# Kernel tuning notes

Measured on AMD Instinct MI355X. Metric: run time of the kernel, lower is better.

## Reference

```python
import jax, jax.numpy as jnp
import numpy as np

SEARCH_RANGE = 4  # max_displacement; kernel_size=1, strides=1, pad=search_range
LEAKY_SLOPE = 0.1


def setup_inputs() -> dict:
    key = jax.random.key(0)
    k1, k2 = jax.random.split(key)
    B, H, W, C = 8, 128, 128, 192
    prv = jax.random.normal(k1, (B, H, W, C), dtype=jnp.float32)
    nxt = jax.random.normal(k2, (B, H, W, C), dtype=jnp.float32)
    return {"prv": prv, "nxt": nxt}


def _cost_volume(prv, nxt, d):
    # tfa CorrelationCost with kernel_size=1: for each displacement (dy, dx) in
    # [-d, d]^2, out[b,y,x,k] = mean_c prv[b,y,x,c] * nxt[b,y+dy,x+dx,c],
    # with zero padding of nxt by d. Displacements ordered row-major (dy outer).
    B, H, W, C = prv.shape
    nxt_p = jnp.pad(nxt, ((0, 0), (d, d), (d, d), (0, 0)))
    outs = []
    for dy in range(2 * d + 1):  # fixed small set (9)
        for dx in range(2 * d + 1):
            shifted = nxt_p[:, dy:dy + H, dx:dx + W, :]  # [B,H,W,C]
            outs.append(jnp.mean(prv * shifted, axis=-1))  # [B,H,W]
    return jnp.stack(outs, axis=-1)  # [B,H,W,81]


def reference(prv, nxt):
    cv = _cost_volume(prv, nxt, SEARCH_RANGE)
    return jax.nn.leaky_relu(cv, LEAKY_SLOPE)
```

## Files before the change

kernel.cpp:

```cpp
#include <hip/hip_runtime.h>
#include <hip/hip_bf16.h>


#define B_ 8
#define H_ 128
#define W_ 128
#define C_ 192
#define ND 9
#define NDISP 81
#define HT 16
#define WT 16
#define KS 32
#define NK 6
#define BROWS 24
#define BCOLS 24
#define APIX (HT * WT)
#define BPIX (BROWS * BCOLS)
#define ASTR 257
#define BSTR 577
#define ASLOTS (8 * ASTR)
#define BSLOTS (8 * BSTR)
#define NSA 2
#define NSB 5

typedef short short8 __attribute__((ext_vector_type(8)));
typedef short short4_t __attribute__((ext_vector_type(4)));
typedef float f32x4 __attribute__((ext_vector_type(4)));

static __device__ __forceinline__ short bf1(float f) {
    __hip_bfloat16 h = __float2bfloat16(f);
    return __builtin_bit_cast(short, h);
}

static __device__ __forceinline__ short4_t cvt4(float4 v) {
    short4_t r;
    r[0] = bf1(v.x); r[1] = bf1(v.y); r[2] = bf1(v.z); r[3] = bf1(v.w);
    return r;
}

static __device__ __forceinline__ short8 cat(short4_t u, short4_t v) {
    return __builtin_shufflevector(u, v, 0, 1, 2, 3, 4, 5, 6, 7);
}

static __device__ __forceinline__ void barrier_no_vm_drain() {
    asm volatile("s_waitcnt lgkmcnt(0)\n\ts_barrier" ::: "memory");
}

__global__ __launch_bounds__(1024, 4)
void cv_mfma(const float* __restrict__ prv, const float* __restrict__ nxt,
             float* __restrict__ out) {
    __shared__ short4_t sm[2][ASLOTS + BSLOTS];

    const int tid = threadIdx.x;
    const int w0 = blockIdx.x * WT;
    const int h0 = blockIdx.y * HT;
    const int b  = blockIdx.z;

    const int lane = tid & 63;
    const int wid  = tid >> 6;
    const int lq = lane & 15;
    const int lc = lane >> 4;

    const int tp = tid >> 3;
    const int c8 = tid & 7;

    int aoff[NSA];
#pragma unroll
    for (int i = 0; i < NSA; ++i) {
        const int p = tp + 128 * i;
        const int r = p >> 4;
        const int pc = p & 15;
        aoff[i] = ((b * H_ + h0 + r) * W_ + w0 + pc) * C_ + c8 * 4;
    }
    int boff[NSB];
    unsigned bmask = 0;
#pragma unroll
    for (int i = 0; i < NSB; ++i) {
        const int p = tp + 128 * i;
        const int row = p / BCOLS;
        const int col = p - row * BCOLS;
        const int gh = h0 - 4 + row;
        const int gw = w0 - 4 + col;
        const bool inb = (p < BPIX) && ((unsigned)gh < (unsigned)H_) && ((unsigned)gw < (unsigned)W_);
        if (inb) bmask |= (1u << i);
        boff[i] = ((b * H_ + (inb ? gh : 0)) * W_ + (inb ? gw : 0)) * C_ + c8 * 4;
    }
    const bool wr4 = (tid < 512);

    float4 xa[NSA], xb[NSB];

#pragma unroll
    for (int i = 0; i < NSA; ++i) xa[i] = *(const float4*)(prv + aoff[i]);
#pragma unroll
    for (int i = 0; i < NSB; ++i) {
        xb[i] = make_float4(0.f, 0.f, 0.f, 0.f);
        if (bmask & (1u << i)) xb[i] = *(const float4*)(nxt + boff[i]);
    }

    f32x4 acc[ND][2];
#pragma unroll
    for (int d = 0; d < ND; ++d) {
        acc[d][0] = (f32x4){0.f, 0.f, 0.f, 0.f};
        acc[d][1] = (f32x4){0.f, 0.f, 0.f, 0.f};
    }

    for (int it = 0; it < NK; ++it) {
        short4_t* sA = sm[it & 1];
        short4_t* sB = sm[it & 1] + ASLOTS;

#pragma unroll
        for (int i = 0; i < NSA; ++i)
            sA[c8 * ASTR + tp + 128 * i] = cvt4(xa[i]);
#pragma unroll
        for (int i = 0; i < NSB - 1; ++i)
            sB[c8 * BSTR + tp + 128 * i] = cvt4(xb[i]);
        if (wr4)
            sB[c8 * BSTR + tp + 128 * (NSB - 1)] = cvt4(xb[NSB - 1]);

        if (it + 1 < NK) {
            const int co = (it + 1) * KS;
#pragma unroll
            for (int i = 0; i < NSA; ++i) xa[i] = *(const float4*)(prv + aoff[i] + co);
#pragma unroll
            for (int i = 0; i < NSB; ++i) {
                if (bmask & (1u << i)) xb[i] = *(const float4*)(nxt + boff[i] + co);
            }
        }

        barrier_no_vm_drain();

        const int pA = wid * WT + lq;
        const short8 a = cat(sA[2 * lc * ASTR + pA], sA[(2 * lc + 1) * ASTR + pA]);
#pragma unroll
        for (int dy = 0; dy < ND; ++dy) {
            const int pB = (wid + dy) * BCOLS + lq;
            const short8 b0 = cat(sB[2 * lc * BSTR + pB],     sB[(2 * lc + 1) * BSTR + pB]);
            const short8 b1 = cat(sB[2 * lc * BSTR + pB + 8], sB[(2 * lc + 1) * BSTR + pB + 8]);
            acc[dy][0] = __builtin_amdgcn_mfma_f32_16x16x32_bf16(a, b0, acc[dy][0], 0, 0, 0);
            acc[dy][1] = __builtin_amdgcn_mfma_f32_16x16x32_bf16(a, b1, acc[dy][1], 0, 0, 0);
        }
    }

    const float inv = 1.0f / (float)C_;
    const int h = h0 + wid;
    if (lc < 2) {
#pragma unroll
        for (int rg = 0; rg < 4; ++rg) {
            const int r = 4 * lc + rg;
            const int dx = lq - r;
            if (dx >= 0 && dx <= 8) {
                float* o = out + (size_t)((b * H_ + h) * W_ + w0 + r) * NDISP + dx;
#pragma unroll
                for (int dy = 0; dy < ND; ++dy) {
                    const float v = acc[dy][0][rg] * inv;
                    o[dy * ND] = v >= 0.f ? v : 0.1f * v;
                }
            }
        }
    } else {
#pragma unroll
        for (int rg = 0; rg < 4; ++rg) {
            const int r = 4 * lc + rg;
            const int dx = lq - r + 8;
            if (dx >= 0 && dx <= 8) {
                float* o = out + (size_t)((b * H_ + h) * W_ + w0 + r) * NDISP + dx;
#pragma unroll
                for (int dy = 0; dy < ND; ++dy) {
                    const float v = acc[dy][1][rg] * inv;
                    o[dy * ND] = v >= 0.f ? v : 0.1f * v;
                }
            }
        }
    }
}

extern "C" void kernel_launch(void* const* d_in, const int* in_sizes, int n_in,
                              void* d_out, int out_size, void* d_ws, size_t ws_size,
                              hipStream_t stream) {
    const float* prv = (const float*)d_in[0];
    const float* nxt = (const float*)d_in[1];
    float* out = (float*)d_out;

    dim3 grid(W_ / WT, H_ / HT, B_);
    cv_mfma<<<grid, 1024, 0, stream>>>(prv, nxt, out);
}
```

Before: 77.50 us.

## Halve spatial tile height and drop register-prefetch double buffering

Shrinks the block tile from 16x16 to 8x16 output pixels with 512 threads, so the nxt halo grows relative to the tile (16x24 loaded per 8 rows instead of 24x24 per 16). It removes the double-buffered LDS with register prefetch and replaces it with a single LDS buffer, loading each channel slice and then synchronising twice per slice. The smaller LDS footprint and block may raise occupancy and the number of blocks, at the cost of more redundant halo traffic and less overlap between global loads and MFMA work.

Result: slower. 110.4 us (+42.4%).

```diff
diff --git a/kernel.cpp b/kernel.cpp
--- a/kernel.cpp
+++ b/kernel.cpp
@@ -8,20 +8,18 @@
 #define C_ 192
 #define ND 9
 #define NDISP 81
-#define HT 16
+#define HT 8
 #define WT 16
 #define KS 32
 #define NK 6
-#define BROWS 24
+#define BROWS 16
 #define BCOLS 24
 #define APIX (HT * WT)
 #define BPIX (BROWS * BCOLS)
-#define ASTR 257
-#define BSTR 577
-#define ASLOTS (8 * ASTR)
-#define BSLOTS (8 * BSTR)
+#define ASTR 129
+#define BSTR 385
 #define NSA 2
-#define NSB 5
+#define NSB 6
 
 typedef short short8 __attribute__((ext_vector_type(8)));
 typedef short short4_t __attribute__((ext_vector_type(4)));
@@ -42,14 +40,12 @@
     return __builtin_shufflevector(u, v, 0, 1, 2, 3, 4, 5, 6, 7);
 }
 
-static __device__ __forceinline__ void barrier_no_vm_drain() {
-    asm volatile("s_waitcnt lgkmcnt(0)\n\ts_barrier" ::: "memory");
-}
-
-__global__ __launch_bounds__(1024, 4)
+__global__ __launch_bounds__(512, 4)
 void cv_mfma(const float* __restrict__ prv, const float* __restrict__ nxt,
              float* __restrict__ out) {
-    __shared__ short4_t sm[2][ASLOTS + BSLOTS];
+    __shared__ short4_t sm[8 * ASTR + 8 * BSTR];
+    short4_t* sA = sm;
+    short4_t* sB = sm + 8 * ASTR;
 
     const int tid = threadIdx.x;
     const int w0 = blockIdx.x * WT;
@@ -67,7 +63,7 @@
     int aoff[NSA];
 #pragma unroll
     for (int i = 0; i < NSA; ++i) {
-        const int p = tp + 128 * i;
+        const int p = tp + 64 * i;
         const int r = p >> 4;
         const int pc = p & 15;
         aoff[i] = ((b * H_ + h0 + r) * W_ + w0 + pc) * C_ + c8 * 4;
@@ -76,25 +72,14 @@
     unsigned bmask = 0;
 #pragma unroll
     for (int i = 0; i < NSB; ++i) {
-        const int p = tp + 128 * i;
+        const int p = tp + 64 * i;
         const int row = p / BCOLS;
         const int col = p - row * BCOLS;
         const int gh = h0 - 4 + row;
         const int gw = w0 - 4 + col;
-        const bool inb = (p < BPIX) && ((unsigned)gh < (unsigned)H_) && ((unsigned)gw < (unsigned)W_);
+        const bool inb = ((unsigned)gh < (unsigned)H_) && ((unsigned)gw < (unsigned)W_);
         if (inb) bmask |= (1u << i);
         boff[i] = ((b * H_ + (inb ? gh : 0)) * W_ + (inb ? gw : 0)) * C_ + c8 * 4;
-    }
-    const bool wr4 = (tid < 512);
-
-    float4 xa[NSA], xb[NSB];
-
-#pragma unroll
-    for (int i = 0; i < NSA; ++i) xa[i] = *(const float4*)(prv + aoff[i]);
-#pragma unroll
-    for (int i = 0; i < NSB; ++i) {
-        xb[i] = make_float4(0.f, 0.f, 0.f, 0.f);
-        if (bmask & (1u << i)) xb[i] = *(const float4*)(nxt + boff[i]);
     }
 
     f32x4 acc[ND][2];
@@ -104,30 +89,29 @@
         acc[d][1] = (f32x4){0.f, 0.f, 0.f, 0.f};
     }
 
-    for (int it = 0; it < NK; ++it) {
-        short4_t* sA = sm[it & 1];
-        short4_t* sB = sm[it & 1] + ASLOTS;
+    for (int ks = 0; ks < NK; ++ks) {
+        if (ks) __syncthreads();
+        const int co = ks * KS;
 
+        {
+            float4 va[NSA];
 #pragma unroll
-        for (int i = 0; i < NSA; ++i)
-            sA[c8 * ASTR + tp + 128 * i] = cvt4(xa[i]);
-#pragma unroll
-        for (int i = 0; i < NSB - 1; ++i)
-            sB[c8 * BSTR + tp + 128 * i] = cvt4(xb[i]);
-        if (wr4)
-            sB[c8 * BSTR + tp + 128 * (NSB - 1)] = cvt4(xb[NSB - 1]);
-
-        if (it + 1 < NK) {
-            const int co = (it + 1) * KS;
-#pragma unroll
-            for (int i = 0; i < NSA; ++i) xa[i] = *(const float4*)(prv + aoff[i] + co);
+            for (int i = 0; i < NSA; ++i)
+                va[i] = *(const float4*)(prv + aoff[i] + co);
+            float4 vb[NSB];
 #pragma unroll
             for (int i = 0; i < NSB; ++i) {
-                if (bmask & (1u << i)) xb[i] = *(const float4*)(nxt + boff[i] + co);
+                vb[i] = make_float4(0.f, 0.f, 0.f, 0.f);
+                if (bmask & (1u << i)) vb[i] = *(const float4*)(nxt + boff[i] + co);
             }
+#pragma unroll
+            for (int i = 0; i < NSA; ++i)
+                sA[c8 * ASTR + tp + 64 * i] = cvt4(va[i]);
+#pragma unroll
+            for (int i = 0; i < NSB; ++i)
+                sB[c8 * BSTR + tp + 64 * i] = cvt4(vb[i]);
         }
-
-        barrier_no_vm_drain();
+        __syncthreads();
 
         const int pA = wid * WT + lq;
         const short8 a = cat(sA[2 * lc * ASTR + pA], sA[(2 * lc + 1) * ASTR + pA]);
@@ -182,5 +166,5 @@
     float* out = (float*)d_out;
 
     dim3 grid(W_ / WT, H_ / HT, B_);
-    cv_mfma<<<grid, 1024, 0, stream>>>(prv, nxt, out);
+    cv_mfma<<<grid, 512, 0, stream>>>(prv, nxt, out);
 }
```
